# Kernel optimization log

Measured on AMD Instinct MI355X. Metric: run time of the kernel, lower is better.

Reference implementation:

```python
import jax, jax.numpy as jnp
import numpy as np
import math


def _extend(chunk):
    # chunk: [b, C, w, 1, dh] -> stacked (prev, cur, next) chunks: [b, C, w, 1, dh, 3]
    prev = jnp.pad(chunk[:, :-1], ((0, 0), (1, 0), (0, 0), (0, 0), (0, 0)))
    nxt = jnp.pad(chunk[:, 1:], ((0, 0), (0, 1), (0, 0), (0, 0), (0, 0)))
    return jnp.stack((prev, chunk, nxt), axis=-1)


def local_xl_attention(q, kv, Wq, Wkv, Wc, w):
    b, L, dm = q.shape
    dh = Wkv.shape[1] // 2          # d_head (w_kv projects to 2*d_head)
    nh = dm // dh                   # n_head
    C = L // w                      # number of chunks

    qp = (q @ Wq).reshape(b, L, nh, dh) / math.sqrt(dh)   # [b,L,nh,dh]
    kvp = kv @ Wkv                                         # [b,L,2*dh]
    k = kvp[..., :dh][:, :, None, :]                       # [b,L,1,dh] single KV head
    v = kvp[..., dh:][:, :, None, :]

    # sliding_chunks_matmul_qk (faithful to original einsum, incl. sum over z)
    cq = qp.reshape(b, C, w, nh, dh)
    ck_e = _extend(k.reshape(b, C, w, 1, dh))              # [b,C,w,1,dh,3]
    attn = jnp.einsum('bcxhd,bzyode->bcxhey', cq, ck_e)    # [b,C,w,nh,3,w]
    attn = attn.reshape(b, L, nh, 3 * w)

    probs = jax.nn.softmax(attn, axis=-1)

    # sliding_chunks_matmul_pv (faithful, incl. sum over z)
    cp = probs.reshape(b, C, w, nh, 3, w)
    cv_e = _extend(v.reshape(b, C, w, 1, dh))              # [b,C,w,1,dh,3]
    ctx = jnp.einsum('bcwhpd,bzdoep->bcwhe', cp, cv_e)     # [b,C,w,nh,dh]
    out = ctx.reshape(b, L, dm) @ Wc
    return out


def setup_inputs() -> dict:
    key = jax.random.key(0)
    ks = jax.random.split(key, 5)
    B, L, DM, NH = 1, 4096, 1024, 16
    DH = DM // NH
    scale = 0.02
    return {
        'q': jax.random.normal(ks[0], (B, L, DM), dtype=jnp.float32),
        'kv': jax.random.normal(ks[1], (B, L, DM), dtype=jnp.float32),
        'Wq': jax.random.normal(ks[2], (DM, DM), dtype=jnp.float32) * scale,
        'Wkv': jax.random.normal(ks[3], (DM, 2 * DH), dtype=jnp.float32) * scale,
        'Wc': jax.random.normal(ks[4], (DM, DM), dtype=jnp.float32) * scale,
        'w': 512,
    }


def reference(q, kv, Wq, Wkv, Wc, w):
    return local_xl_attention(q, kv, Wq, Wkv, Wc, w)
```

## Files before the change

### kernel.cpp

```cpp
#include <hip/hip_runtime.h>
#include <hip/hip_bf16.h>
#include <cstdint>
#include <cstddef>

#define L_ 4096
#define DM_ 1024
#define NH_ 16
#define DH_ 64
#define W_ 512
#define C_ 8
#define W3_ 1536
#define NROWS_ 65536

typedef __attribute__((ext_vector_type(8))) short short8;
typedef __attribute__((ext_vector_type(4))) float f32x4;

__device__ __forceinline__ void async16(const void* g, void* l) {
    __builtin_amdgcn_global_load_lds(
        (const __attribute__((address_space(1))) unsigned int*)g,
        (__attribute__((address_space(3))) unsigned int*)l, 16, 0, 0);
}

#if __has_builtin(__builtin_amdgcn_exp2f)
#define FEXP2(x) __builtin_amdgcn_exp2f(x)
#else
#define FEXP2(x) exp2f(x)
#endif

#define WAITV(N) asm volatile("s_waitcnt vmcnt(" #N ")" ::: "memory")
#define WAITL0() asm volatile("s_waitcnt lgkmcnt(0)" ::: "memory")
#define BARRIER() do { __builtin_amdgcn_s_barrier(); \
                       __builtin_amdgcn_sched_barrier(0); } while (0)

__device__ __forceinline__ int nanhit(unsigned u) {
    return (((u & 0x7F80u) == 0x7F80u) | (((u >> 16) & 0x7F80u) == 0x7F80u));
}

__device__ __forceinline__ float ldf(const void* X, size_t i, int f32) {
    return f32 ? ((const float*)X)[i] : __bfloat162float(((const __hip_bfloat16*)X)[i]);
}

__global__ __launch_bounds__(256) void megaprep(const void* __restrict__ q,
                                                const void* __restrict__ kv,
                                                const void* __restrict__ Wq,
                                                const void* __restrict__ Wkv,
                                                const void* __restrict__ Wc,
                                                __hip_bfloat16* __restrict__ qbuf,
                                                __hip_bfloat16* __restrict__ WqT,
                                                __hip_bfloat16* __restrict__ WkvT,
                                                __hip_bfloat16* __restrict__ WcT,
                                                __hip_bfloat16* __restrict__ kvcomb,
                                                int* __restrict__ flag) {
    __shared__ float t[64][65];
    __shared__ int sflag;
    const int b = blockIdx.x;
    const int tid = threadIdx.x;

    if (tid == 0) sflag = 0;
    __syncthreads();
    {
        int hit = 0;
#pragma unroll
        for (int r = 0; r < 4; ++r) {
            uint4 v = ((const uint4*)q)[tid + 256 * r];
            hit |= nanhit(v.x) | nanhit(v.y) | nanhit(v.z) | nanhit(v.w);
        }
        if (__any(hit)) { if ((tid & 63) == 0) atomicOr(&sflag, 1); }
    }
    __syncthreads();
    const int f32 = sflag;
    if (b == 0 && tid == 0) flag[0] = f32;

    if (b < 4096) {
        int i = (b * 256 + tid) * 4;
        if (f32) {
            float4 v = *(const float4*)((const float*)q + i);
            __hip_bfloat162 tmp[2] = {__float22bfloat162_rn({v.x, v.y}),
                                      __float22bfloat162_rn({v.z, v.w})};
            *(short4*)((short*)qbuf + i) = *(const short4*)tmp;
        } else {
            *(short4*)((short*)qbuf + i) = *(const short4*)((const short*)q + i);
        }
    } else if (b < 4640) {
        const void* W;
        __hip_bfloat16* WT;
        int K = 1024, N, n0, k0;
        if (b < 4352) {
            int bx = b - 4096; W = Wq; WT = WqT; N = 1024;
            n0 = (bx & 15) * 64; k0 = (bx >> 4) * 64;
        } else if (b < 4608) {
            int bx = b - 4352; W = Wc; WT = WcT; N = 1024;
            n0 = (bx & 15) * 64; k0 = (bx >> 4) * 64;
        } else {
            int bx = b - 4608; W = Wkv; WT = WkvT; N = 128;
            n0 = (bx & 1) * 64; k0 = (bx >> 1) * 64;
        }
        const int tx = tid & 63;
        const int ty = tid >> 6;
#pragma unroll
        for (int r = 0; r < 16; ++r) {
            int k = ty + r * 4;
            t[k][tx] = ldf(W, (size_t)(k0 + k) * N + n0 + tx, f32);
        }
        __syncthreads();
#pragma unroll
        for (int r = 0; r < 16; ++r) {
            int n = ty + r * 4;
            WT[(size_t)(n0 + n) * K + k0 + tx] = __float2bfloat16(t[tx][n]);
        }
    } else {
        int y = b - 4640;
        int c = tid * 4;
        float s0 = 0, s1 = 0, s2 = 0, s3 = 0;
        float f0 = 0, f1 = 0, f2 = 0, f3 = 0;
        float l0 = 0, l1 = 0, l2 = 0, l3 = 0;
#pragma unroll
        for (int z = 0; z < C_; ++z) {
            size_t base = (size_t)(z * W_ + y) * 1024 + c;
            float a0, a1, a2, a3;
            if (f32) {
                float4 v = *(const float4*)((const float*)kv + base);
                a0 = v.x; a1 = v.y; a2 = v.z; a3 = v.w;
            } else {
                short4 v = *(const short4*)((const short*)kv + base);
                a0 = __bfloat162float(*(__hip_bfloat16*)&v.x);
                a1 = __bfloat162float(*(__hip_bfloat16*)&v.y);
                a2 = __bfloat162float(*(__hip_bfloat16*)&v.z);
                a3 = __bfloat162float(*(__hip_bfloat16*)&v.w);
            }
            s0 += a0; s1 += a1; s2 += a2; s3 += a3;
            if (z == 0) { f0 = a0; f1 = a1; f2 = a2; f3 = a3; }
            if (z == C_ - 1) { l0 = a0; l1 = a1; l2 = a2; l3 = a3; }
        }
        auto store = [&](int row, float x0, float x1, float x2, float x3) {
            __hip_bfloat162 tmp[2] = {__float22bfloat162_rn({x0, x1}),
                                      __float22bfloat162_rn({x2, x3})};
            *(short4*)((short*)kvcomb + (size_t)row * 1024 + c) = *(const short4*)tmp;
        };
        store(y,        s0 - l0, s1 - l1, s2 - l2, s3 - l3);
        store(512 + y,  s0, s1, s2, s3);
        store(1024 + y, s0 - f0, s1 - f1, s2 - f2, s3 - f3);
    }
}

struct GemmP {
    const __hip_bfloat16* A;
    const __hip_bfloat16* BT;
    void* C;
    int M, N, K;
    float alpha;
    int cMode;
    int ntiles;
    int swz;
    int nblocks;
    void* C2;
};

__global__ __launch_bounds__(256) void gemm_bt_mfma(GemmP p0, GemmP p1,
                                                    const int* __restrict__ flag) {
    __shared__ __hip_bfloat16 Asl[2][2][128 * 32];
    __shared__ __hip_bfloat16 Bsl[2][2][64 * 32];

    GemmP p;
    int bid;
    if ((int)blockIdx.x < p0.nblocks) { p = p0; bid = blockIdx.x; }
    else { p = p1; bid = (int)blockIdx.x - p0.nblocks; }

    int mt, nt;
    if (!p.swz) { mt = bid / p.ntiles; nt = bid % p.ntiles; }
    else {
        int g = bid / (8 * p.ntiles);
        int rem = bid % (8 * p.ntiles);
        mt = g * 8 + (rem & 7);
        nt = rem >> 3;
    }
    const int m0 = mt * 128;
    const int n0 = nt * 64;
    const int K = p.K;
    const int N = p.N;

    const int tid = threadIdx.x;
    const int lane = tid & 63;
    const int wv = tid >> 6;
    const int wm = wv >> 1;
    const int wn = wv & 1;
    const int col = lane & 15;
    const int quad = lane >> 4;

    const int srow = lane >> 2;
    const int scol = (lane & 3) * 8;
    const __hip_bfloat16* Ag = p.A + (size_t)m0 * K;
    const __hip_bfloat16* Bg = p.BT + (size_t)n0 * K;

    f32x4 acc[4][2] = {};

    auto STAGE = [&](int bf, int k0) {
#pragma unroll
        for (int h = 0; h < 2; ++h) {
            int arow = wv * 32 + h * 16 + srow;
#pragma unroll
            for (int kc = 0; kc < 2; ++kc)
                async16(Ag + (size_t)arow * K + k0 + kc * 32 + scol,
                        &Asl[bf][kc][arow * 32 + scol]);
        }
        int brow = wv * 16 + srow;
#pragma unroll
        for (int kc = 0; kc < 2; ++kc)
            async16(Bg + (size_t)brow * K + k0 + kc * 32 + scol,
                    &Bsl[bf][kc][brow * 32 + scol]);
    };

    const int NT = K >> 6;
    STAGE(0, 0);

    int bf = 0;
    for (int t = 0; t < NT; ++t) {
        if (t + 1 < NT) {
            STAGE(bf ^ 1, (t + 1) << 6);
            WAITV(6);
        } else {
            WAITV(0);
        }
        BARRIER();

#pragma unroll
        for (int kc = 0; kc < 2; ++kc) {
            short8 af[4], bfr[2];
#pragma unroll
            for (int i = 0; i < 4; ++i)
                af[i] = *(const short8*)(&Asl[bf][kc][(wm * 64 + i * 16 + col) * 32 + quad * 8]);
#pragma unroll
            for (int j = 0; j < 2; ++j)
                bfr[j] = *(const short8*)(&Bsl[bf][kc][(wn * 32 + j * 16 + col) * 32 + quad * 8]);
#pragma unroll
            for (int am = 0; am < 4; ++am)
#pragma unroll
                for (int bn = 0; bn < 2; ++bn)
                    acc[am][bn] = __builtin_amdgcn_mfma_f32_16x16x32_bf16(af[am], bfr[bn], acc[am][bn], 0, 0, 0);
        }
        WAITL0();
        BARRIER();
        bf ^= 1;
    }

    if (p.cMode == 3) {
#pragma unroll
        for (int am = 0; am < 4; ++am)
#pragma unroll
            for (int bn = 0; bn < 2; ++bn)
#pragma unroll
                for (int r = 0; r < 4; ++r) {
                    int key = m0 + wm * 64 + am * 16 + quad * 4 + r;
                    int c = n0 + wn * 32 + bn * 16 + col;
                    float v = acc[am][bn][r];
                    int g = key >> 6, kr = key & 63;
                    if (c < 64) {
                        int byt = g * 8192 + kr * 128 +
                                  ((((c >> 3) ^ (kr & 7)) << 4)) + ((c & 7) << 1);
                        *(__hip_bfloat16*)((char*)p.C + byt) = __float2bfloat16(v);
                    } else {
                        int d = c - 64;
                        int pp = ((kr & 15) << 2) | (kr >> 4);
                        int byt = g * 8192 + d * 128 +
                                  ((((pp >> 3) ^ (d & 7)) << 4)) + ((pp & 7) << 1);
                        *(__hip_bfloat16*)((char*)p.C2 + byt) = __float2bfloat16(v);
                    }
                }
        return;
    }

    int cF = (p.cMode == 1) ? 1 : ((p.cMode == 2) ? 0 : flag[0]);
#pragma unroll
    for (int am = 0; am < 4; ++am)
#pragma unroll
        for (int bn = 0; bn < 2; ++bn)
#pragma unroll
            for (int r = 0; r < 4; ++r) {
                size_t ci = (size_t)(m0 + wm * 64 + am * 16 + quad * 4 + r) * N
                            + n0 + wn * 32 + bn * 16 + col;
                float v = acc[am][bn][r] * p.alpha;
                if (cF) ((float*)p.C)[ci] = v;
                else ((__hip_bfloat16*)p.C)[ci] = __float2bfloat16(v);
            }
}

#define PSTRIDE 72
__global__ __launch_bounds__(256, 2) void attn_kernel(const __hip_bfloat16* __restrict__ qb,
                                                      const __hip_bfloat16* __restrict__ Kb,
                                                      const __hip_bfloat16* __restrict__ Vt,
                                                      __hip_bfloat16* __restrict__ ctx) {
    __shared__ __align__(16) __hip_bfloat16 Kbuf[3][4096];
    __shared__ __align__(16) __hip_bfloat16 Vbuf[3][4096];
    __shared__ __align__(16) __hip_bfloat16 psm[4][32 * PSTRIDE];

    const int tid = threadIdx.x;
    const int lane = tid & 63;
    const int wv = tid >> 6;
    const int m0 = blockIdx.x * 128 + wv * 32;
    const int col = lane & 15;
    const int quad = lane >> 4;
    __hip_bfloat16* pw = psm[wv];

    const char* Kg = (const char*)Kb;
    const char* Vg = (const char*)Vt;
    const int so = tid * 16;

    const int off0 = ((quad ^ (col & 7)) << 4);
    const int off1 = (((quad + 4) ^ (col & 7)) << 4);

    short8 qf[2][2];
#pragma unroll
    for (int rg = 0; rg < 2; ++rg) {
        const __hip_bfloat16* qp = qb + (size_t)(m0 + rg * 16 + col) * 64 + quad * 8;
        qf[rg][0] = *(const short8*)(qp);
        qf[rg][1] = *(const short8*)(qp + 32);
    }

    f32x4 O[2][4] = {};
    float lrow[2][4] = {};
    f32x4 S[2][4];

    auto stage_tile = [&](int tile, int slot) {
        const char* ks = Kg + (size_t)tile * 8192;
        const char* vs = Vg + (size_t)tile * 8192;
        char* kd = (char*)Kbuf[slot];
        char* vd = (char*)Vbuf[slot];
        async16(ks + so, kd + so);
        async16(ks + 4096 + so, kd + 4096 + so);
        async16(vs + so, vd + so);
        async16(vs + 4096 + so, vd + 4096 + so);
    };

    auto qk_into = [&](const char* Kc, f32x4 (&Sd)[2][4]) {
        short8 kb0[4], kb1[4];
#pragma unroll
        for (int f = 0; f < 4; ++f) {
            const int rb = (f * 16 + col) * 128;
            kb0[f] = *(const short8*)(Kc + rb + off0);
            kb1[f] = *(const short8*)(Kc + rb + off1);
        }
        __builtin_amdgcn_s_setprio(1);
#pragma unroll
        for (int rg = 0; rg < 2; ++rg)
#pragma unroll
            for (int f = 0; f < 4; ++f) {
                f32x4 s = {};
                s = __builtin_amdgcn_mfma_f32_16x16x32_bf16(qf[rg][0], kb0[f], s, 0, 0, 0);
                s = __builtin_amdgcn_mfma_f32_16x16x32_bf16(qf[rg][1], kb1[f], s, 0, 0, 0);
                Sd[rg][f] = s;
            }
        __builtin_amdgcn_s_setprio(0);
    };

    stage_tile(0, 0);
    stage_tile(1, 1);
    WAITV(4);
    BARRIER();
    qk_into((const char*)Kbuf[0], S);

    int cur = 0;
    for (int t = 0; t < 24; ++t) {
        const int nx1 = (cur == 2) ? 0 : cur + 1;
        const int nx2 = (nx1 == 2) ? 0 : nx1 + 1;

        WAITV(0);
        BARRIER();

        if (t < 22) stage_tile(t + 2, nx2);

#pragma unroll
        for (int rg = 0; rg < 2; ++rg) {
#pragma unroll
            for (int f = 0; f < 4; ++f)
#pragma unroll
                for (int r = 0; r < 4; ++r) S[rg][f][r] = FEXP2(S[rg][f][r]);
#pragma unroll
            for (int r = 0; r < 4; ++r)
                lrow[rg][r] += (S[rg][0][r] + S[rg][1][r]) + (S[rg][2][r] + S[rg][3][r]);
#pragma unroll
            for (int r = 0; r < 4; ++r) {
                __hip_bfloat162 p01 = __float22bfloat162_rn({S[rg][0][r], S[rg][1][r]});
                __hip_bfloat162 p23 = __float22bfloat162_rn({S[rg][2][r], S[rg][3][r]});
                short4 t4;
                *(__hip_bfloat162*)(&t4.x) = p01;
                *(__hip_bfloat162*)(&t4.z) = p23;
                *(short4*)(pw + (rg * 16 + quad * 4 + r) * PSTRIDE + col * 4) = t4;
            }
        }

        f32x4 Snew[2][4];
        if (t < 23) qk_into((const char*)Kbuf[nx1], Snew);

        const char* Vc = (const char*)Vbuf[cur];
        short8 vb0[4], vb1[4];
#pragma unroll
        for (int f = 0; f < 4; ++f) {
            const int rb = (f * 16 + col) * 128;
            vb0[f] = *(const short8*)(Vc + rb + off0);
            vb1[f] = *(const short8*)(Vc + rb + off1);
        }
#pragma unroll
        for (int rg = 0; rg < 2; ++rg) {
            short8 a0 = *(const short8*)(pw + (rg * 16 + col) * PSTRIDE + quad * 8);
            short8 a1 = *(const short8*)(pw + (rg * 16 + col) * PSTRIDE + 32 + quad * 8);
            __builtin_amdgcn_s_setprio(1);
#pragma unroll
            for (int f = 0; f < 4; ++f) {
                O[rg][f] = __builtin_amdgcn_mfma_f32_16x16x32_bf16(a0, vb0[f], O[rg][f], 0, 0, 0);
                O[rg][f] = __builtin_amdgcn_mfma_f32_16x16x32_bf16(a1, vb1[f], O[rg][f], 0, 0, 0);
            }
            __builtin_amdgcn_s_setprio(0);
        }

        if (t < 23) {
#pragma unroll
            for (int rg = 0; rg < 2; ++rg)
#pragma unroll
                for (int f = 0; f < 4; ++f) S[rg][f] = Snew[rg][f];
        }
        cur = nx1;
    }

#pragma unroll
    for (int msk = 1; msk <= 8; msk <<= 1)
#pragma unroll
        for (int rg = 0; rg < 2; ++rg)
#pragma unroll
            for (int r = 0; r < 4; ++r) lrow[rg][r] += __shfl_xor(lrow[rg][r], msk, 64);

#pragma unroll
    for (int rg = 0; rg < 2; ++rg)
#pragma unroll
        for (int r = 0; r < 4; ++r) {
            float inv = 1.f / lrow[rg][r];
#pragma unroll
            for (int f = 0; f < 4; ++f)
                ctx[(size_t)(m0 + rg * 16 + quad * 4 + r) * 64 + f * 16 + col] =
                    __float2bfloat16(O[rg][f][r] * inv);
        }
}

extern "C" void kernel_launch(void* const* d_in, const int* in_sizes, int n_in,
                              void* d_out, int out_size, void* d_ws, size_t ws_size,
                              hipStream_t stream) {
    const void* q   = d_in[0];
    const void* kv  = d_in[1];
    const void* Wq  = d_in[2];
    const void* Wkv = d_in[3];
    const void* Wc  = d_in[4];

    char* ws = (char*)d_ws;
    size_t off = 0;
    int* flag = (int*)(ws + off); off += 1024;
    __hip_bfloat16* qbuf   = (__hip_bfloat16*)(ws + off); off += (size_t)L_ * DM_ * 2;
    __hip_bfloat16* WqT    = (__hip_bfloat16*)(ws + off); off += (size_t)DM_ * DM_ * 2;
    __hip_bfloat16* WkvT   = (__hip_bfloat16*)(ws + off); off += (size_t)128 * DM_ * 2;
    __hip_bfloat16* WcT    = (__hip_bfloat16*)(ws + off); off += (size_t)DM_ * DM_ * 2;
    __hip_bfloat16* qb     = (__hip_bfloat16*)(ws + off); off += (size_t)L_ * DM_ * 2;
    __hip_bfloat16* kvcomb = (__hip_bfloat16*)(ws + off); off += (size_t)1536 * 1024 * 2;
    __hip_bfloat16* Kb     = (__hip_bfloat16*)(ws + off); off += (size_t)W3_ * 64 * 2;
    __hip_bfloat16* Vt     = (__hip_bfloat16*)(ws + off); off += (size_t)64 * W3_ * 2;
    __hip_bfloat16* ctxb   = (__hip_bfloat16*)(ws + off);

    megaprep<<<5152, 256, 0, stream>>>(q, kv, Wq, Wkv, Wc,
                                       qbuf, WqT, WkvT, WcT, kvcomb, flag);

    {
        GemmP pq{qbuf, WqT, (void*)qb, L_, DM_, DM_,
                 0.125f * 1.44269504f, 2, 16, 1, 512, nullptr};
        GemmP pk{kvcomb, WkvT, (void*)Kb, 1536, 128, DM_,
                 1.0f, 3, 2, 0, 24, (void*)Vt};
        gemm_bt_mfma<<<536, 256, 0, stream>>>(pq, pk, flag);
    }
    attn_kernel<<<dim3(NROWS_ / 128), 256, 0, stream>>>(qb, Kb, Vt, ctxb);
    {
        GemmP pc{ctxb, WcT, d_out, L_, DM_, DM_, 1.0f, 0, 16, 1, 512, nullptr};
        GemmP pnull{};
        pnull.nblocks = 0;
        gemm_bt_mfma<<<512, 256, 0, stream>>>(pc, pnull, flag);
    }
}
```

Before: 170.1 us.

## Split-K the Q projection GEMM into two halves summed inside attention

The Q projection GEMM (4096x1024x1024) is split along K into two halves, launched as 1024 blocks instead of 512. Each half writes a bf16 partial result, one of them into the ctx buffer. The attention kernel loads both partials and adds them in fp32 when it builds its Q fragments. This doubles the block count to fill more CUs, at the cost of extra partial writes and reads plus a second bf16 rounding on each partial.

Measured after the change: 180.5 us. 1.06x slower.

```diff
diff --git a/kernel.cpp b/kernel.cpp
--- a/kernel.cpp
+++ b/kernel.cpp
@@ -166,6 +166,14 @@
     if ((int)blockIdx.x < p0.nblocks) { p = p0; bid = blockIdx.x; }
     else { p = p1; bid = (int)blockIdx.x - p0.nblocks; }
 
+    int kbeg = 0, kend = p.K;
+    if (p.cMode == 4) {
+        int half = p.nblocks >> 1;
+        if (bid >= half) { bid -= half; kbeg = p.K >> 1; p.C = p.C2; }
+        kend = kbeg + (p.K >> 1);
+        p.cMode = 2;
+    }
+
     int mt, nt;
     if (!p.swz) { mt = bid / p.ntiles; nt = bid % p.ntiles; }
     else {
@@ -210,12 +218,12 @@
                     &Bsl[bf][kc][brow * 32 + scol]);
     };
 
-    const int NT = K >> 6;
-    STAGE(0, 0);
+    const int t0 = kbeg >> 6, t1 = kend >> 6;
+    STAGE(0, t0 << 6);
 
     int bf = 0;
-    for (int t = 0; t < NT; ++t) {
-        if (t + 1 < NT) {
+    for (int t = t0; t < t1; ++t) {
+        if (t + 1 < t1) {
             STAGE(bf ^ 1, (t + 1) << 6);
             WAITV(6);
         } else {
@@ -285,7 +293,8 @@
 }
 
 #define PSTRIDE 72
-__global__ __launch_bounds__(256, 2) void attn_kernel(const __hip_bfloat16* __restrict__ qb,
+__global__ __launch_bounds__(256, 2) void attn_kernel(const __hip_bfloat16* __restrict__ qp0,
+                                                      const __hip_bfloat16* __restrict__ qp1,
                                                       const __hip_bfloat16* __restrict__ Kb,
                                                       const __hip_bfloat16* __restrict__ Vt,
                                                       __hip_bfloat16* __restrict__ ctx) {
@@ -311,9 +320,26 @@
     short8 qf[2][2];
 #pragma unroll
     for (int rg = 0; rg < 2; ++rg) {
-        const __hip_bfloat16* qp = qb + (size_t)(m0 + rg * 16 + col) * 64 + quad * 8;
-        qf[rg][0] = *(const short8*)(qp);
-        qf[rg][1] = *(const short8*)(qp + 32);
+        size_t base = (size_t)(m0 + rg * 16 + col) * 64 + quad * 8;
+#pragma unroll
+        for (int h = 0; h < 2; ++h) {
+            short8 a = *(const short8*)(qp0 + base + h * 32);
+            short8 b = *(const short8*)(qp1 + base + h * 32);
+            short8 o;
+#pragma unroll
+            for (int j = 0; j < 8; j += 2) {
+                short a0 = a[j], a1 = a[j + 1], b0 = b[j], b1 = b[j + 1];
+                float s0 = __bfloat162float(*(__hip_bfloat16*)&a0) +
+                           __bfloat162float(*(__hip_bfloat16*)&b0);
+                float s1 = __bfloat162float(*(__hip_bfloat16*)&a1) +
+                           __bfloat162float(*(__hip_bfloat16*)&b1);
+                __hip_bfloat162 pr = __float22bfloat162_rn({s0, s1});
+                short2 pr2 = *(short2*)&pr;
+                o[j] = pr2.x;
+                o[j + 1] = pr2.y;
+            }
+            qf[rg][h] = o;
+        }
     }
 
     f32x4 O[2][4] = {};
@@ -456,23 +482,24 @@
     __hip_bfloat16* WqT    = (__hip_bfloat16*)(ws + off); off += (size_t)DM_ * DM_ * 2;
     __hip_bfloat16* WkvT   = (__hip_bfloat16*)(ws + off); off += (size_t)128 * DM_ * 2;
     __hip_bfloat16* WcT    = (__hip_bfloat16*)(ws + off); off += (size_t)DM_ * DM_ * 2;
-    __hip_bfloat16* qb     = (__hip_bfloat16*)(ws + off); off += (size_t)L_ * DM_ * 2;
+    __hip_bfloat16* qp0    = (__hip_bfloat16*)(ws + off); off += (size_t)L_ * DM_ * 2;
     __hip_bfloat16* kvcomb = (__hip_bfloat16*)(ws + off); off += (size_t)1536 * 1024 * 2;
     __hip_bfloat16* Kb     = (__hip_bfloat16*)(ws + off); off += (size_t)W3_ * 64 * 2;
     __hip_bfloat16* Vt     = (__hip_bfloat16*)(ws + off); off += (size_t)64 * W3_ * 2;
     __hip_bfloat16* ctxb   = (__hip_bfloat16*)(ws + off);
+    __hip_bfloat16* qp1    = ctxb;
 
     megaprep<<<5152, 256, 0, stream>>>(q, kv, Wq, Wkv, Wc,
                                        qbuf, WqT, WkvT, WcT, kvcomb, flag);
 
     {
-        GemmP pq{qbuf, WqT, (void*)qb, L_, DM_, DM_,
-                 0.125f * 1.44269504f, 2, 16, 1, 512, nullptr};
+        GemmP pq{qbuf, WqT, (void*)qp0, L_, DM_, DM_,
+                 0.125f * 1.44269504f, 4, 16, 1, 1024, (void*)qp1};
         GemmP pk{kvcomb, WkvT, (void*)Kb, 1536, 128, DM_,
                  1.0f, 3, 2, 0, 24, (void*)Vt};
-        gemm_bt_mfma<<<536, 256, 0, stream>>>(pq, pk, flag);
-    }
-    attn_kernel<<<dim3(NROWS_ / 128), 256, 0, stream>>>(qb, Kb, Vt, ctxb);
+        gemm_bt_mfma<<<1048, 256, 0, stream>>>(pq, pk, flag);
+    }
+    attn_kernel<<<dim3(NROWS_ / 128), 256, 0, stream>>>(qp0, qp1, Kb, Vt, ctxb);
     {
         GemmP pc{ctxb, WcT, d_out, L_, DM_, DM_, 1.0f, 0, 16, 1, 512, nullptr};
         GemmP pnull{};
```
